# Kernel tuning notes

Measured on AMD Instinct MI355X. Metric: run time of the kernel, lower is better.

The kernel has to match this reference:

```python
import math
import jax, jax.numpy as jnp
import numpy as np

B, S, D, H, DFF = 4, 2048, 1024, 16, 4096
DK = D // H
EPS = 1e-6


def setup_inputs() -> dict:
    key = jax.random.key(0)
    ks = jax.random.split(key, 12)
    w = lambda k, sh: jax.random.normal(k, sh, dtype=jnp.float32) * 0.02
    return {
        "x": jax.random.normal(ks[0], (B, S, D), dtype=jnp.float32),
        "mask": jax.random.randint(ks[1], (B, 1, S, S), 0, 2, dtype=jnp.int32),
        "ln1_a": jnp.ones((D,), jnp.float32), "ln1_b": jnp.zeros((D,), jnp.float32),
        "Wq": w(ks[2], (D, D)), "bq": jnp.zeros((D,), jnp.float32),
        "Wk": w(ks[3], (D, D)), "bk": jnp.zeros((D,), jnp.float32),
        "Wv": w(ks[4], (D, D)), "bv": jnp.zeros((D,), jnp.float32),
        "Wo": w(ks[5], (D, D)), "bo": jnp.zeros((D,), jnp.float32),
        "ln2_a": jnp.ones((D,), jnp.float32), "ln2_b": jnp.zeros((D,), jnp.float32),
        "W1": w(ks[6], (D, DFF)), "b1": jnp.zeros((DFF,), jnp.float32),
        "W2": w(ks[7], (DFF, D)), "b2": jnp.zeros((D,), jnp.float32),
    }


def layernorm(x, a, b):
    # BERT4REC LayerNorm: unbiased std (ddof=1), eps added to std (not var)
    mean = jnp.mean(x, axis=-1, keepdims=True)
    std = jnp.std(x, axis=-1, keepdims=True, ddof=1)
    return a * (x - mean) / (std + EPS) + b


def gelu_tanh(x):
    c = math.sqrt(2.0 / math.pi)
    return 0.5 * x * (1.0 + jnp.tanh(c * (x + 0.044715 * x * x * x)))


def reference(x, mask, ln1_a, ln1_b, Wq, bq, Wk, bk, Wv, bv, Wo, bo,
              ln2_a, ln2_b, W1, b1, W2, b2):
    xb = layernorm(x, ln1_a, ln1_b)
    # multi-head attention (dropout off / eval mode)
    q = (xb @ Wq + bq).reshape(B, S, H, DK).transpose(0, 2, 1, 3)
    k = (xb @ Wk + bk).reshape(B, S, H, DK).transpose(0, 2, 1, 3)
    v = (xb @ Wv + bv).reshape(B, S, H, DK).transpose(0, 2, 1, 3)
    scores = jnp.einsum("bhqd,bhkd->bhqk", q, k) / math.sqrt(DK)
    scores = jnp.where(mask == 0, jnp.float32(-1e9), scores)
    p = jax.nn.softmax(scores, axis=-1)
    attn = jnp.einsum("bhqk,bhkd->bhqd", p, v)
    attn = attn.transpose(0, 2, 1, 3).reshape(B, S, D)
    x = x + (attn @ Wo + bo)
    # FFN sublayer
    xb = layernorm(x, ln2_a, ln2_b)
    ff = gelu_tanh(xb @ W1 + b1) @ W2 + b2
    return x + ff
```

## Files before the change

kernel.cpp:

```cpp
#include <hip/hip_runtime.h>

#define Bb 4
#define Ss 2048
#define Dd 1024
#define Hh 16
#define DFF 4096

typedef unsigned short u16;
typedef __attribute__((ext_vector_type(8))) short v8s;
typedef __attribute__((ext_vector_type(4))) float v4f;
typedef __attribute__((ext_vector_type(4))) unsigned short v4u16;
typedef __attribute__((ext_vector_type(4))) unsigned v4u;

__device__ __forceinline__ u16 f2bf(float f) {
  unsigned u = __builtin_bit_cast(unsigned, f);
  return (u16)((u + 0x7fffu + ((u >> 16) & 1u)) >> 16);
}

__device__ __forceinline__ unsigned cvtpk(float a, float b) {
  unsigned r;
  asm("v_cvt_pk_bf16_f32 %0, %1, %2" : "=v"(r) : "v"(a), "v"(b));
  return r;
}

__device__ __forceinline__ void gload16(const void* g, void* l) {
  __builtin_amdgcn_global_load_lds((const __attribute__((address_space(1))) unsigned*)g,
                                   (__attribute__((address_space(3))) unsigned*)l, 16, 0, 0);
}

__device__ __forceinline__ v4f mfma16(v8s a, v8s b, v4f c) {
  return __builtin_amdgcn_mfma_f32_16x16x32_bf16(a, b, c, 0, 0, 0);
}

__device__ __forceinline__ float fexp2_raw(float s) {
  const int i = (int)__builtin_fmaf(s, 8388608.0f, 1064998378.0f);
  return __builtin_bit_cast(float, i);
}

__device__ __forceinline__ float gelu_f(float x) {
  float y = 0.7978845608028654f * (x + 0.044715f * x * x * x);
  y = fminf(fmaxf(y, -15.f), 15.f);
  float t = 1.0f - 2.0f / (__expf(2.0f * y) + 1.0f);
  return 0.5f * x * (1.0f + t);
}

__global__ __launch_bounds__(256)
void ln_k(const float* __restrict__ x, const float* __restrict__ ga,
          const float* __restrict__ gb, u16* __restrict__ out) {
  const int row = blockIdx.x, tid = threadIdx.x;
  const float4 v = ((const float4*)(x + (size_t)row * 1024))[tid];
  float s = v.x + v.y + v.z + v.w;
  float q = v.x * v.x + v.y * v.y + v.z * v.z + v.w * v.w;
  #pragma unroll
  for (int o = 1; o < 64; o <<= 1) { s += __shfl_xor(s, o); q += __shfl_xor(q, o); }
  __shared__ float red[8];
  if ((tid & 63) == 0) { red[tid >> 6] = s; red[4 + (tid >> 6)] = q; }
  __syncthreads();
  s = red[0] + red[1] + red[2] + red[3];
  q = red[4] + red[5] + red[6] + red[7];
  const float mean = s * (1.0f / 1024.0f);
  const float var = fmaxf((q - 1024.0f * mean * mean) * (1.0f / 1023.0f), 0.0f);
  const float inv = 1.0f / (sqrtf(var) + 1e-6f);
  const int c0 = tid * 4;
  u16* o4 = out + (size_t)row * 1024 + c0;
  const float vv[4] = {v.x, v.y, v.z, v.w};
  #pragma unroll
  for (int i = 0; i < 4; i++)
    o4[i] = f2bf(ga[c0 + i] * (vv[i] - mean) * inv + gb[c0 + i]);
}

__global__ __launch_bounds__(256)
void wt_k(const float* __restrict__ w, u16* __restrict__ wt, int K, int N) {
  __shared__ float tile[32 * 33];
  const int t = threadIdx.x;
  const int k0 = blockIdx.x << 5, n0 = blockIdx.y << 5;
  {
    const int r = t >> 3, c4 = (t & 7) << 2;
    const float4 v = *(const float4*)&w[(size_t)(k0 + r) * N + n0 + c4];
    tile[r * 33 + c4 + 0] = v.x; tile[r * 33 + c4 + 1] = v.y;
    tile[r * 33 + c4 + 2] = v.z; tile[r * 33 + c4 + 3] = v.w;
  }
  __syncthreads();
  {
    const int r = t >> 3, c4 = (t & 7) << 2;
    v4u16 uv;
    #pragma unroll
    for (int i = 0; i < 4; i++) uv[i] = f2bf(tile[(c4 + i) * 33 + r]);
    *(v4u16*)&wt[(size_t)(n0 + r) * K + k0 + c4] = uv;
  }
}

__global__ void bcat_k(const float* bq, const float* bk, const float* bv, float* dst) {
  int i = blockIdx.x * 256 + threadIdx.x;
  dst[i] = i < 1024 ? bq[i] : (i < 2048 ? bk[i - 1024] : bv[i - 2048]);
}

__global__ __launch_bounds__(256)
void mask_k(const int* __restrict__ mask, unsigned* __restrict__ mw) {
  const size_t w = (size_t)blockIdx.x * 256 + threadIdx.x;
  const int4* p = (const int4*)(mask + w * 32);
  unsigned bits = 0;
  #pragma unroll
  for (int k = 0; k < 8; k++) {
    const int4 v = p[k];
    bits |= (v.x != 0 ? 1u : 0u) << (k * 4 + 0);
    bits |= (v.y != 0 ? 1u : 0u) << (k * 4 + 1);
    bits |= (v.z != 0 ? 1u : 0u) << (k * 4 + 2);
    bits |= (v.w != 0 ? 1u : 0u) << (k * 4 + 3);
  }
  mw[w] = bits;
}

__global__ __launch_bounds__(256)
void vt_k(const u16* __restrict__ qkv, u16* __restrict__ vt) {
  __shared__ __align__(16) u16 tile[64 * 72];
  const int t = threadIdx.x;
  const int bh = blockIdx.y, b = bh >> 4, h = bh & 15;
  const size_t s0 = (size_t)blockIdx.x * 64;
  {
    const int row = t >> 2, c0 = (t & 3) << 4;
    const u16* src = &qkv[((size_t)b * Ss + s0 + row) * 3072 + 2048 + h * 64 + c0];
    *(v8s*)&tile[row * 72 + c0] = *(const v8s*)src;
    *(v8s*)&tile[row * 72 + c0 + 8] = *(const v8s*)(src + 8);
  }
  __syncthreads();
  {
    const int dk = t >> 2, sc0 = (t & 3) << 4;
    u16* dst = &vt[((size_t)bh * 64 + dk) * Ss + s0 + sc0];
    v4u16 a, bvv, cvv, d;
    #pragma unroll
    for (int i = 0; i < 4; i++) a[i] = tile[(sc0 + i) * 72 + dk];
    #pragma unroll
    for (int i = 0; i < 4; i++) bvv[i] = tile[(sc0 + 4 + i) * 72 + dk];
    #pragma unroll
    for (int i = 0; i < 4; i++) cvv[i] = tile[(sc0 + 8 + i) * 72 + dk];
    #pragma unroll
    for (int i = 0; i < 4; i++) d[i] = tile[(sc0 + 12 + i) * 72 + dk];
    *(v4u16*)(dst + 0) = a; *(v4u16*)(dst + 4) = bvv;
    *(v4u16*)(dst + 8) = cvv; *(v4u16*)(dst + 12) = d;
  }
}

template<int EPI>
__global__ __launch_bounds__(256, 3)
void gemm_bt(const u16* __restrict__ A, const u16* __restrict__ Bt,
             const float* __restrict__ bias, const float* res,
             void* out, int M, int N, int K) {
  __shared__ __align__(16) u16 lA[2][128 * 32];
  __shared__ __align__(16) u16 lB[2][128 * 32];
  const int tid = threadIdx.x;
  const int lane = tid & 63, wid = tid >> 6;
  const int c = lane & 15, g = lane >> 4;
  const int nt = N >> 7;
  const int nwg = gridDim.x;
  const int bid0 = blockIdx.x;
  const int bid = (bid0 & 7) * (nwg >> 3) + (bid0 >> 3);
  const int bm = bid / nt, bn = bid - bm * nt;
  const int row0 = bm << 7, col0 = bn << 7;
  const int wr = (wid >> 1) << 6, wc = (wid & 1) << 6;

  v4f acc[4][4] = {};

  const int arow = tid >> 2, ak = (tid & 3) << 3;
  const u16* gA = A + (size_t)(row0 + arow) * K + ak;
  const u16* gB = Bt + (size_t)(col0 + arow) * K + ak;
  const int ldo = wid * 512;
  const size_t rstep = (size_t)64 * K;

  for (int kt = 0; kt < K; kt += 64) {
    __syncthreads();
    #pragma unroll
    for (int s = 0; s < 2; s++) {
      const int ks = kt + s * 32;
      gload16(gA + ks, &lA[s][ldo]);
      gload16(gA + ks + rstep, &lA[s][ldo + 2048]);
      gload16(gB + ks, &lB[s][ldo]);
      gload16(gB + ks + rstep, &lB[s][ldo + 2048]);
    }
    __syncthreads();
    #pragma unroll
    for (int s = 0; s < 2; s++) {
      v8s af[4], bfr[4];
      #pragma unroll
      for (int m = 0; m < 4; m++) af[m] = *(const v8s*)&lA[s][(wr + m * 16 + c) * 32 + g * 8];
      #pragma unroll
      for (int n = 0; n < 4; n++) bfr[n] = *(const v8s*)&lB[s][(wc + n * 16 + c) * 32 + g * 8];
      #pragma unroll
      for (int m = 0; m < 4; m++)
        #pragma unroll
        for (int n = 0; n < 4; n++)
          acc[m][n] = mfma16(af[m], bfr[n], acc[m][n]);
    }
  }

  float bv[4];
  #pragma unroll
  for (int n = 0; n < 4; n++) bv[n] = bias[col0 + wc + n * 16 + c];
  #pragma unroll
  for (int m = 0; m < 4; m++) {
    #pragma unroll
    for (int n = 0; n < 4; n++) {
      #pragma unroll
      for (int j = 0; j < 4; j++) {
        const int r = row0 + wr + m * 16 + g * 4 + j;
        const int cc = col0 + wc + n * 16 + c;
        const size_t idx = (size_t)r * N + cc;
        const float v = acc[m][n][j] + bv[n];
        if constexpr (EPI == 0) ((u16*)out)[idx] = f2bf(v);
        else if constexpr (EPI == 1) ((float*)out)[idx] = res[idx] + v;
        else ((u16*)out)[idx] = f2bf(gelu_f(v));
      }
    }
  }
}

__global__ __launch_bounds__(256, 4)
void attn_k(const u16* __restrict__ qkv, const u16* __restrict__ vt,
            const unsigned* __restrict__ mw, u16* __restrict__ ctx) {
  __shared__ __align__(16) u16 lK[128 * 64];
  __shared__ __align__(16) u16 lV[64 * 128];

  const int tid = threadIdx.x, lane = tid & 63, wid = tid >> 6;
  const int c = lane & 15, g = lane >> 4;
  const bool b4 = (lane & 16) != 0;
  const int bid = blockIdx.x;
  const int swz = (bid & 7) * 128 + (bid >> 3);
  const int bh = swz >> 4, qb = swz & 15;
  const int b = bh >> 4, h = bh & 15;
  const int qw = (qb << 7) + wid * 32;

  v8s qs[2][2];
  #pragma unroll
  for (int m = 0; m < 2; m++)
    #pragma unroll
    for (int ks = 0; ks < 2; ks++) {
      const v8s q = *(const v8s*)&qkv[((size_t)b * Ss + qw + m * 16 + c) * 3072 + h * 64 + ks * 32 + g * 8];
      v4u w;
      #pragma unroll
      for (int p = 0; p < 4; p++) {
        const float a = __builtin_bit_cast(float, (unsigned)((u16)q[2 * p]) << 16) * 0.18033688f;
        const float e = __builtin_bit_cast(float, (unsigned)((u16)q[2 * p + 1]) << 16) * 0.18033688f;
        w[p] = cvtpk(a, e);
      }
      qs[m][ks] = __builtin_bit_cast(v8s, w);
    }

  v4f o[2][4] = {};
  float ls[2] = {0.f, 0.f};

  const unsigned* mrow0 = mw + ((size_t)b * Ss + qw + c) * 64;

  const int skey = tid >> 3;
  const int kchunk = (((tid & 7) ^ ((tid >> 3) & 7)) << 3);
  const int vdk = tid >> 4;
  const int vchunk = (((tid & 15) ^ ((tid >> 4) & 15)) << 3);
  const u16* gK = &qkv[((size_t)b * Ss + skey) * 3072 + 1024 + h * 64 + kchunk];
  const u16* gV = &vt[((size_t)bh * 64 + vdk) * Ss + vchunk];
  u16* const dK = &lK[(wid * 8) * 64];
  u16* const dV = &lV[(wid * 4) * 128];

  for (int kt = 0; kt < 16; kt++) {
    __syncthreads();
    #pragma unroll
    for (int i = 0; i < 4; i++) {
      gload16(gK + ((size_t)kt * 128 + i * 32) * 3072, dK + i * (32 * 64));
      gload16(gV + (size_t)(i * 16) * Ss + kt * 128, dV + i * (16 * 128));
    }
    __syncthreads();

    #pragma unroll
    for (int m = 0; m < 2; m++) {
      v4f sc[8] = {};
      __builtin_amdgcn_s_setprio(1);
      #pragma unroll
      for (int f = 0; f < 8; f++) {
        const v8s k0 = *(const v8s*)&lK[(f * 16 + c) * 64 + ((g ^ (c & 7)) << 3)];
        const v8s k1 = *(const v8s*)&lK[(f * 16 + c) * 64 + (((g + 4) ^ (c & 7)) << 3)];
        sc[f] = mfma16(k0, qs[m][0], sc[f]);
        sc[f] = mfma16(k1, qs[m][1], sc[f]);
      }
      __builtin_amdgcn_s_setprio(0);
      const uint4 mv = *(const uint4*)(mrow0 + (size_t)m * 16 * 64 + kt * 4);
      const unsigned mvw[4] = {mv.x, mv.y, mv.z, mv.w};
      float rs = 0.f;
      #pragma unroll
      for (int f = 0; f < 8; f++) {
        const unsigned bits = mvw[f >> 1] >> (((f & 1) << 4) + (g << 2));
        #pragma unroll
        for (int j = 0; j < 4; j++) {
          const float sm = ((bits >> j) & 1u) ? sc[f][j] : -126.0f;
          const float p = fexp2_raw(sm);
          sc[f][j] = p;
          rs += p;
        }
      }
      rs += __shfl_xor(rs, 16);
      {
        unsigned ru = __builtin_bit_cast(unsigned, rs), rv = ru;
        asm("v_permlane32_swap_b32 %0, %1" : "+v"(ru), "+v"(rv));
        rs = __builtin_bit_cast(float, ru) + __builtin_bit_cast(float, rv);
      }
      ls[m] += rs;
      unsigned p0[8], p1[8];
      #pragma unroll
      for (int f = 0; f < 8; f++) {
        p0[f] = cvtpk(sc[f][0], sc[f][1]);
        p1[f] = cvtpk(sc[f][2], sc[f][3]);
      }
      __builtin_amdgcn_s_setprio(1);
      #pragma unroll
      for (int kk = 0; kk < 4; kk++) {
        unsigned X0 = p0[2 * kk],     X1 = p1[2 * kk];
        unsigned Y0 = p0[2 * kk + 1], Y1 = p1[2 * kk + 1];
        asm("v_permlane32_swap_b32 %0, %1" : "+v"(Y0), "+v"(X0));
        asm("v_permlane32_swap_b32 %0, %1" : "+v"(Y1), "+v"(X1));
        const unsigned A0 = b4 ? (unsigned)__shfl_xor((int)Y0, 16) : X0;
        const unsigned A1 = b4 ? (unsigned)__shfl_xor((int)Y1, 16) : X1;
        const unsigned B0 = b4 ? Y0 : (unsigned)__shfl_xor((int)X0, 16);
        const unsigned B1 = b4 ? Y1 : (unsigned)__shfl_xor((int)X1, 16);
        uint4 t4; t4.x = A0; t4.y = A1; t4.z = B0; t4.w = B1;
        const v8s a8 = __builtin_bit_cast(v8s, t4);
        #pragma unroll
        for (int n = 0; n < 4; n++) {
          const v8s vb = *(const v8s*)&lV[(n * 16 + c) * 128 + (((kk * 4 + g) ^ c) << 3)];
          o[m][n] = mfma16(a8, vb, o[m][n]);
        }
      }
      __builtin_amdgcn_s_setprio(0);
    }
  }

  #pragma unroll
  for (int m = 0; m < 2; m++) {
    #pragma unroll
    for (int j = 0; j < 4; j++) {
      const float lsj = __shfl(ls[m], (g << 2) + j);
      const float inv = lsj > 0.f ? 1.0f / lsj : 0.f;
      const size_t row = (size_t)b * Ss + qw + m * 16 + (g << 2) + j;
      #pragma unroll
      for (int n = 0; n < 4; n++)
        ctx[row * Dd + h * 64 + n * 16 + c] = f2bf(o[m][n][j] * inv);
    }
  }
}

extern "C" void kernel_launch(void* const* d_in, const int* in_sizes, int n_in,
                              void* d_out, int out_size, void* d_ws, size_t ws_size,
                              hipStream_t stream) {
  const float* x    = (const float*)d_in[0];
  const int*   mask = (const int*)d_in[1];
  const float* ln1a = (const float*)d_in[2];
  const float* ln1b = (const float*)d_in[3];
  const float* Wq   = (const float*)d_in[4];
  const float* bq   = (const float*)d_in[5];
  const float* Wk   = (const float*)d_in[6];
  const float* bk   = (const float*)d_in[7];
  const float* Wv   = (const float*)d_in[8];
  const float* bv   = (const float*)d_in[9];
  const float* Wo   = (const float*)d_in[10];
  const float* bo   = (const float*)d_in[11];
  const float* ln2a = (const float*)d_in[12];
  const float* ln2b = (const float*)d_in[13];
  const float* W1   = (const float*)d_in[14];
  const float* b1   = (const float*)d_in[15];
  const float* W2   = (const float*)d_in[16];
  const float* b2   = (const float*)d_in[17];
  float* out = (float*)d_out;

  char* ws = (char*)d_ws;
  u16* wqkvT    = (u16*)(ws);
  u16* woT      = (u16*)(ws + 6291456);
  u16* w1T      = (u16*)(ws + 8388608);
  u16* w2T      = (u16*)(ws + 16777216);
  float* bqkv   = (float*)(ws + 25165824);
  unsigned* mw  = (unsigned*)(ws + 25178112);
  u16* xb       = (u16*)(ws + 27275264);
  u16* qkv      = (u16*)(ws + 44052480);
  u16* h1       = qkv;
  u16* vt       = (u16*)(ws + 111161344);
  u16* ctx      = (u16*)(ws + 127938560);

  wt_k<<<dim3(32, 32),  256, 0, stream>>>(Wq, wqkvT,           1024, 1024);
  wt_k<<<dim3(32, 32),  256, 0, stream>>>(Wk, wqkvT + 1048576, 1024, 1024);
  wt_k<<<dim3(32, 32),  256, 0, stream>>>(Wv, wqkvT + 2097152, 1024, 1024);
  wt_k<<<dim3(32, 32),  256, 0, stream>>>(Wo, woT,             1024, 1024);
  wt_k<<<dim3(32, 128), 256, 0, stream>>>(W1, w1T,             1024, 4096);
  wt_k<<<dim3(128, 32), 256, 0, stream>>>(W2, w2T,             4096, 1024);
  bcat_k<<<12, 256, 0, stream>>>(bq, bk, bv, bqkv);
  mask_k<<<2048, 256, 0, stream>>>(mask, mw);
  ln_k<<<8192, 256, 0, stream>>>(x, ln1a, ln1b, xb);

  gemm_bt<0><<<64 * 24, 256, 0, stream>>>(xb, wqkvT, bqkv, nullptr, qkv, 8192, 3072, 1024);
  vt_k<<<dim3(32, 64), 256, 0, stream>>>(qkv, vt);
  attn_k<<<1024, 256, 0, stream>>>(qkv, vt, mw, ctx);
  gemm_bt<1><<<64 * 8, 256, 0, stream>>>(ctx, woT, bo, x, out, 8192, 1024, 1024);
  ln_k<<<8192, 256, 0, stream>>>(out, ln2a, ln2b, xb);
  gemm_bt<2><<<64 * 32, 256, 0, stream>>>(xb, w1T, b1, nullptr, h1, 8192, 4096, 1024);
  gemm_bt<1><<<64 * 8, 256, 0, stream>>>(h1, w2T, b2, out, out, 8192, 1024, 4096);
}
```

Baseline: 473.6 us.

## Double-buffer GEMM LDS tiles to overlap global loads with MFMA compute

Restructures the bf16 GEMM main loop into a two-buffer LDS pipeline. The next 32-wide K slab is issued with direct global-to-LDS loads while the current slab feeds the MFMAs, with one vmcnt wait and barrier per step. The old loop loaded a 64-wide K block, waited, then computed, so the load latency was exposed. The trade-off is twice as many barrier points per unit of K and less compute per step to hide each load behind.

```diff
diff --git a/kernel.cpp b/kernel.cpp
--- a/kernel.cpp
+++ b/kernel.cpp
@@ -166,30 +166,39 @@
   const u16* gB = Bt + (size_t)(col0 + arow) * K + ak;
   const int ldo = wid * 512;
   const size_t rstep = (size_t)64 * K;
-
-  for (int kt = 0; kt < K; kt += 64) {
-    __syncthreads();
-    #pragma unroll
-    for (int s = 0; s < 2; s++) {
-      const int ks = kt + s * 32;
-      gload16(gA + ks, &lA[s][ldo]);
-      gload16(gA + ks + rstep, &lA[s][ldo + 2048]);
-      gload16(gB + ks, &lB[s][ldo]);
-      gload16(gB + ks + rstep, &lB[s][ldo + 2048]);
-    }
-    __syncthreads();
-    #pragma unroll
-    for (int s = 0; s < 2; s++) {
-      v8s af[4], bfr[4];
-      #pragma unroll
-      for (int m = 0; m < 4; m++) af[m] = *(const v8s*)&lA[s][(wr + m * 16 + c) * 32 + g * 8];
-      #pragma unroll
-      for (int n = 0; n < 4; n++) bfr[n] = *(const v8s*)&lB[s][(wc + n * 16 + c) * 32 + g * 8];
-      #pragma unroll
-      for (int m = 0; m < 4; m++)
-        #pragma unroll
-        for (int n = 0; n < 4; n++)
-          acc[m][n] = mfma16(af[m], bfr[n], acc[m][n]);
+  const int NT = K >> 5;
+
+  auto stage = [&](int t, int buf) {
+    const int ks = t << 5;
+    gload16(gA + ks, &lA[buf][ldo]);
+    gload16(gA + ks + rstep, &lA[buf][ldo + 2048]);
+    gload16(gB + ks, &lB[buf][ldo]);
+    gload16(gB + ks + rstep, &lB[buf][ldo + 2048]);
+  };
+
+  stage(0, 0);
+  asm volatile("s_waitcnt vmcnt(0)" ::: "memory");
+  __builtin_amdgcn_s_barrier();
+  asm volatile("" ::: "memory");
+
+  int cur = 0;
+  for (int t = 0; t < NT; t++) {
+    if (t + 1 < NT) stage(t + 1, cur ^ 1);
+    v8s af[4], bfr[4];
+    #pragma unroll
+    for (int m = 0; m < 4; m++) af[m] = *(const v8s*)&lA[cur][(wr + m * 16 + c) * 32 + g * 8];
+    #pragma unroll
+    for (int n = 0; n < 4; n++) bfr[n] = *(const v8s*)&lB[cur][(wc + n * 16 + c) * 32 + g * 8];
+    #pragma unroll
+    for (int m = 0; m < 4; m++)
+      #pragma unroll
+      for (int n = 0; n < 4; n++)
+        acc[m][n] = mfma16(af[m], bfr[n], acc[m][n]);
+    if (t + 1 < NT) {
+      asm volatile("s_waitcnt vmcnt(0)" ::: "memory");
+      __builtin_amdgcn_s_barrier();
+      asm volatile("" ::: "memory");
+      cur ^= 1;
     }
   }
 
```

Measured after the change: 490.3 us. 3.5% more time.
